# Kernel optimization log

Hardware: AMD Instinct MI355X
Metric: run time of the kernel (lower is better)

The kernel has to match this reference:

```python
import jax, jax.numpy as jnp
import numpy as np

DIM = 512
NUM_HEADS = 8
HEAD_DIM = DIM // NUM_HEADS
SCALE = HEAD_DIM ** -0.5


def setup_inputs() -> dict:
    key = jax.random.key(0)
    ks = jax.random.split(key, 5)
    B, N = 4, 2048
    x = jax.random.normal(ks[0], (B, N, DIM), dtype=jnp.float32)
    # Learned parameters (torch nn.Linear style: y = x @ W.T + b)
    w_qkv = jax.random.normal(ks[1], (3 * DIM, DIM), dtype=jnp.float32) * (DIM ** -0.5)
    b_qkv = jnp.zeros((3 * DIM,), dtype=jnp.float32)
    w_proj = jax.random.normal(ks[2], (DIM, DIM), dtype=jnp.float32) * (DIM ** -0.5)
    b_proj = jnp.zeros((DIM,), dtype=jnp.float32)
    return {"x": x, "w_qkv": w_qkv, "b_qkv": b_qkv, "w_proj": w_proj, "b_proj": b_proj}


def reference(x, w_qkv, b_qkv, w_proj, b_proj):
    B, N, C = x.shape
    qkv = x @ w_qkv.T + b_qkv                      # [B, N, 3C]
    qkv = qkv.reshape(B, N, 3, NUM_HEADS, HEAD_DIM)
    qkv = jnp.transpose(qkv, (2, 0, 3, 1, 4))      # [3, B, H, N, d]
    q, k, v = qkv[0], qkv[1], qkv[2]
    attn = jnp.einsum("bhqd,bhkd->bhqk", q, k) * SCALE  # [B, H, N, N]
    attn = jax.nn.softmax(attn, axis=-1)
    out = jnp.einsum("bhqk,bhkd->bhqd", attn, v)   # [B, H, N, d]
    out = jnp.transpose(out, (0, 2, 1, 3)).reshape(B, N, C)
    return out @ w_proj.T + b_proj
```

## Files before the change

### kernel.cpp

```cpp
#include <hip/hip_runtime.h>

#define DIM 512
#define NHEAD 8
#define HDIM 64
#define BATCH 4
#define SEQ 2048
#define MTOT (BATCH*SEQ)
#define SCALE 0.125f
#define LOG2E 1.4426950408889634f

typedef __bf16 bf16_t;
typedef __bf16 bf16x8 __attribute__((ext_vector_type(8)));
typedef __bf16 bf16x4 __attribute__((ext_vector_type(4)));
typedef __bf16 bf16x2 __attribute__((ext_vector_type(2)));
typedef float f32x4 __attribute__((ext_vector_type(4)));

#define ASYNC_COPY16(g, l) __builtin_amdgcn_global_load_lds( \
    (const __attribute__((address_space(1))) void*)(g),      \
    (__attribute__((address_space(3))) void*)(l), 16, 0, 0)

#define NX_ELEM  (4194304)
#define NWQ_ELEM (786432)
#define NWP_ELEM (262144)
__global__ __launch_bounds__(256) void cvt_kernel(const float* __restrict__ x,
                                                  const float* __restrict__ wq,
                                                  const float* __restrict__ wp,
                                                  bf16_t* __restrict__ out) {
    int i = (blockIdx.x * 256 + threadIdx.x) * 4;
    const float* src;
    if (i < NX_ELEM)                 src = x  + i;
    else if (i < NX_ELEM + NWQ_ELEM) src = wq + (i - NX_ELEM);
    else                             src = wp + (i - NX_ELEM - NWQ_ELEM);
    float4 v = *reinterpret_cast<const float4*>(src);
    bf16x4 o;
    o[0] = (bf16_t)v.x; o[1] = (bf16_t)v.y; o[2] = (bf16_t)v.z; o[3] = (bf16_t)v.w;
    *reinterpret_cast<bf16x4*>(out + i) = o;
}

__global__ __launch_bounds__(256) void gemm_qkv_kernel(
    const bf16_t* __restrict__ X, const bf16_t* __restrict__ W,
    const float* __restrict__ bias,
    bf16_t* __restrict__ Qo, bf16_t* __restrict__ Ko, bf16_t* __restrict__ Vto)
{
    __shared__ bf16_t smem[16384];
    bf16_t (*As)[64] = reinterpret_cast<bf16_t (*)[64]>(smem);
    bf16_t (*Bs)[64] = reinterpret_cast<bf16_t (*)[64]>(smem + 8192);
    unsigned int* Lw = reinterpret_cast<unsigned int*>(smem);
    const int tid = threadIdx.x;
    const int wave = tid >> 6, lane = tid & 63;
    const int lhi = lane >> 4, llo = lane & 15;
    const int o = blockIdx.x;
    const int x = o & 7, i0 = o >> 3;
    const int m0 = (x * 8 + (i0 & 7)) * 128;
    const int n0 = (i0 >> 3) * 128;
    const int wr = (wave >> 1) * 64, wc = (wave & 1) * 64;
    f32x4 acc[4][4] = {};

    const int srow = wave * 32 + (lane >> 3);
    const int scol = (lane & 7) * 8;
    const bf16_t* gA = X + (size_t)(m0 + srow) * DIM + scol;
    const bf16_t* gB = W + (size_t)(n0 + srow) * DIM + scol;

    for (int k0 = 0; k0 < DIM; k0 += 64) {
        #pragma unroll
        for (int p = 0; p < 4; ++p) {
            ASYNC_COPY16(gA + (size_t)p * 8 * DIM + k0, &As[wave*32 + p*8][0]);
            ASYNC_COPY16(gB + (size_t)p * 8 * DIM + k0, &Bs[wave*32 + p*8][0]);
        }
        __syncthreads();
        #pragma unroll
        for (int ks = 0; ks < 2; ++ks) {
            bf16x8 af[4], bfr[4];
            #pragma unroll
            for (int i = 0; i < 4; ++i)
                af[i] = *reinterpret_cast<const bf16x8*>(&As[wr + i*16 + llo][ks*32 + lhi*8]);
            #pragma unroll
            for (int j = 0; j < 4; ++j)
                bfr[j] = *reinterpret_cast<const bf16x8*>(&Bs[wc + j*16 + llo][ks*32 + lhi*8]);
            __builtin_amdgcn_s_setprio(1);
            #pragma unroll
            for (int i = 0; i < 4; ++i)
                #pragma unroll
                for (int j = 0; j < 4; ++j)
                    acc[i][j] = __builtin_amdgcn_mfma_f32_16x16x32_bf16(af[i], bfr[j], acc[i][j], 0, 0, 0);
            __builtin_amdgcn_s_setprio(0);
        }
        __syncthreads();
    }

    const int b = m0 >> 11, ns0 = m0 & 2047;

    if (n0 < 1024) {
        const float qscale = (n0 < 512) ? (SCALE * LOG2E) : 1.0f;
        bf16_t* __restrict__ dst = (n0 < 512) ? Qo : Ko;
        #pragma unroll
        for (int j = 0; j < 4; ++j) {
            int ddc = wc + j*16 + llo;
            float bv = bias[n0 + ddc];
            #pragma unroll
            for (int i = 0; i < 4; ++i)
                #pragma unroll
                for (int r = 0; r < 4; ++r) {
                    int ml = wr + i*16 + lhi*4 + r;
                    smem[ml * 128 + (ddc ^ (((ml >> 2) & 3) * 16))] =
                        (bf16_t)((acc[i][j][r] + bv) * qscale);
                }
        }
        __syncthreads();
        #pragma unroll
        for (int k = 0; k < 8; ++k) {
            int c = tid + k * 256;
            int row = c >> 4, colc = (c & 15) * 8;
            uint4 val = *reinterpret_cast<const uint4*>(
                &smem[row * 128 + (colc ^ (((row >> 2) & 3) * 16))]);
            int col = n0 + colc;
            int hh = (col >> 6) & 7, dd = col & 63;
            size_t bh = (size_t)(b * NHEAD + hh);
            *reinterpret_cast<uint4*>(dst + (bh * SEQ + ns0 + row) * HDIM + dd) = val;
        }
    } else {
        #pragma unroll
        for (int j = 0; j < 4; ++j) {
            int ddc = wc + j*16 + llo;
            float bv = bias[n0 + ddc];
            int xsw = (ddc & 7) * 4;
            #pragma unroll
            for (int i = 0; i < 4; ++i) {
                int dwb = (wr >> 1) + i*8 + lhi*2;
                #pragma unroll
                for (int r2 = 0; r2 < 2; ++r2) {
                    bf16x2 t;
                    t[0] = (bf16_t)(acc[i][j][2*r2]     + bv);
                    t[1] = (bf16_t)(acc[i][j][2*r2 + 1] + bv);
                    Lw[ddc * 64 + ((dwb + r2) ^ xsw)] = __builtin_bit_cast(unsigned int, t);
                }
            }
        }
        __syncthreads();
        const int hh_base = (n0 - 1024) >> 6;
        const int chunk = tid & 15;
        #pragma unroll
        for (int rd = 0; rd < 8; ++rd) {
            int ddc = rd * 16 + (tid >> 4);
            uint4 val = *reinterpret_cast<const uint4*>(
                &Lw[ddc * 64 + ((chunk * 4) ^ ((ddc & 7) * 4))]);
            int dd = ddc & 63;
            int hh = hh_base + (ddc >> 6);
            size_t bh = (size_t)(b * NHEAD + hh);
            *reinterpret_cast<uint4*>(Vto + (bh * HDIM + dd) * SEQ + ns0 + chunk * 8) = val;
        }
    }
}

__global__ __launch_bounds__(256, 2) void attn_kernel(
    const bf16_t* __restrict__ Q, const bf16_t* __restrict__ K,
    const bf16_t* __restrict__ Vt, bf16_t* __restrict__ O)
{
    __shared__ bf16_t Ks[2][64][64];
    __shared__ bf16_t Vs[2][64][64];
    const int tid = threadIdx.x;
    const int wave = tid >> 6, lane = tid & 63;
    const int lhi = lane >> 4, llo = lane & 15;
    const int o = blockIdx.x;
    const int w = (o & 7) * 64 + (o >> 3);
    const int qt = w & 15, bh = w >> 4;
    const bf16_t* Qb = Q + (size_t)bh * SEQ * HDIM;
    const bf16_t* Kb = K + (size_t)bh * SEQ * HDIM;
    const bf16_t* Vb = Vt + (size_t)bh * HDIM * SEQ;
    const int q0 = qt * 128 + wave * 32;

    const int ksr = tid >> 3, kg = tid & 7;
    const int kcol = (kg * 8) ^ ((ksr & 7) * 8);
    const int vd = tid >> 3, vg = tid & 7;
    const int pkA = (32*(vg>>2) + 8*((2*vg)&3)   + 4*((vg>>1)&1)) ^ ((vd & 7) * 8);
    const int pkB = (32*(vg>>2) + 8*((2*vg+1)&3) + 4*((vg>>1)&1)) ^ ((vd & 7) * 8);

    bf16x8 aq[2][2];
    #pragma unroll
    for (int qb = 0; qb < 2; ++qb)
        #pragma unroll
        for (int ks = 0; ks < 2; ++ks)
            aq[qb][ks] = *reinterpret_cast<const bf16x8*>(
                Qb + (size_t)(q0 + qb*16 + llo) * HDIM + ks*32 + lhi*8);

    bf16x8 ones;
    #pragma unroll
    for (int e = 0; e < 8; ++e) ones[e] = (bf16_t)1.0f;

    f32x4 acc_o[2][4] = {};
    f32x4 acc_l[2] = {};
    float mstat[2];
    const float THR = 8.0f * LOG2E;
    const int NT = SEQ / 64;

    uint4 kreg0, kreg1, vreg0, vreg1;
    bf16x8 apA[2][2], apB[2][2];
    bf16x8 bvA[2][4], bvB[2][4];

    auto vmax4 = [](const f32x4& v) {
        return fmaxf(fmaxf(v[0], v[1]), fmaxf(v[2], v[3]));
    };

    kreg0 = *reinterpret_cast<const uint4*>(Kb + (size_t)ksr * HDIM + kg*8);
    kreg1 = *reinterpret_cast<const uint4*>(Kb + (size_t)(ksr + 32) * HDIM + kg*8);
    vreg0 = *reinterpret_cast<const uint4*>(Vb + (size_t)vd * SEQ + vg*8);
    vreg1 = *reinterpret_cast<const uint4*>(Vb + (size_t)(vd + 32) * SEQ + vg*8);
    *reinterpret_cast<uint4*>(&Ks[0][ksr][kcol]) = kreg0;
    *reinterpret_cast<uint4*>(&Ks[0][ksr + 32][kcol]) = kreg1;
    *reinterpret_cast<uint2*>(&Vs[0][vd][pkA]) = make_uint2(vreg0.x, vreg0.y);
    *reinterpret_cast<uint2*>(&Vs[0][vd][pkB]) = make_uint2(vreg0.z, vreg0.w);
    *reinterpret_cast<uint2*>(&Vs[0][vd + 32][pkA]) = make_uint2(vreg1.x, vreg1.y);
    *reinterpret_cast<uint2*>(&Vs[0][vd + 32][pkB]) = make_uint2(vreg1.z, vreg1.w);
    __syncthreads();

    kreg0 = *reinterpret_cast<const uint4*>(Kb + (size_t)(64 + ksr) * HDIM + kg*8);
    kreg1 = *reinterpret_cast<const uint4*>(Kb + (size_t)(64 + ksr + 32) * HDIM + kg*8);
    vreg0 = *reinterpret_cast<const uint4*>(Vb + (size_t)vd * SEQ + 64 + vg*8);
    vreg1 = *reinterpret_cast<const uint4*>(Vb + (size_t)(vd + 32) * SEQ + 64 + vg*8);

    {
        f32x4 s[2][4] = {};
        __builtin_amdgcn_s_setprio(1);
        #pragma unroll
        for (int kb = 0; kb < 4; ++kb)
            #pragma unroll
            for (int ks = 0; ks < 2; ++ks) {
                bf16x8 kf = *reinterpret_cast<const bf16x8*>(
                    &Ks[0][kb*16 + llo][(ks*32 + lhi*8) ^ ((llo & 7) * 8)]);
                #pragma unroll
                for (int qb = 0; qb < 2; ++qb)
                    s[qb][kb] = __builtin_amdgcn_mfma_f32_16x16x32_bf16(kf, aq[qb][ks], s[qb][kb], 0, 0, 0);
            }
        __builtin_amdgcn_s_setprio(0);
        #pragma unroll
        for (int qb = 0; qb < 2; ++qb) {
            float mx = fmaxf(fmaxf(vmax4(s[qb][0]), vmax4(s[qb][1])),
                             fmaxf(vmax4(s[qb][2]), vmax4(s[qb][3])));
            mx = fmaxf(mx, __shfl_xor(mx, 16, 64));
            mx = fmaxf(mx, __shfl_xor(mx, 32, 64));
            mstat[qb] = mx;
            #pragma unroll
            for (int kp = 0; kp < 2; ++kp)
                #pragma unroll
                for (int j = 0; j < 4; ++j) {
                    apA[qb][kp][j]     = (bf16_t)__builtin_amdgcn_exp2f(s[qb][2*kp][j]     - mx);
                    apA[qb][kp][4 + j] = (bf16_t)__builtin_amdgcn_exp2f(s[qb][2*kp + 1][j] - mx);
                }
        }
        #pragma unroll
        for (int kp = 0; kp < 2; ++kp)
            #pragma unroll
            for (int qb = 0; qb < 2; ++qb)
                acc_l[qb] = __builtin_amdgcn_mfma_f32_16x16x32_bf16(apA[qb][kp], ones, acc_l[qb], 0, 0, 0);
        #pragma unroll
        for (int kp = 0; kp < 2; ++kp)
            #pragma unroll
            for (int db = 0; db < 4; ++db)
                bvA[kp][db] = *reinterpret_cast<const bf16x8*>(
                    &Vs[0][db*16 + llo][(kp*32 + lhi*8) ^ ((llo & 7) * 8)]);
        *reinterpret_cast<uint4*>(&Ks[1][ksr][kcol]) = kreg0;
        *reinterpret_cast<uint4*>(&Ks[1][ksr + 32][kcol]) = kreg1;
        *reinterpret_cast<uint2*>(&Vs[1][vd][pkA]) = make_uint2(vreg0.x, vreg0.y);
        *reinterpret_cast<uint2*>(&Vs[1][vd][pkB]) = make_uint2(vreg0.z, vreg0.w);
        *reinterpret_cast<uint2*>(&Vs[1][vd + 32][pkA]) = make_uint2(vreg1.x, vreg1.y);
        *reinterpret_cast<uint2*>(&Vs[1][vd + 32][pkB]) = make_uint2(vreg1.z, vreg1.w);
        __syncthreads();
    }

    auto body = [&](int kt, bf16x8 (&apIn)[2][2], bf16x8 (&bvIn)[2][4],
                    bf16x8 (&apOut)[2][2], bf16x8 (&bvOut)[2][4]) {
        const int cur = kt & 1, nxt = cur ^ 1;
        if (kt + 1 < NT) {
            const size_t koff = (size_t)(kt + 1) * 64;
            kreg0 = *reinterpret_cast<const uint4*>(Kb + (koff + ksr) * HDIM + kg*8);
            kreg1 = *reinterpret_cast<const uint4*>(Kb + (koff + ksr + 32) * HDIM + kg*8);
            vreg0 = *reinterpret_cast<const uint4*>(Vb + (size_t)vd * SEQ + koff + vg*8);
            vreg1 = *reinterpret_cast<const uint4*>(Vb + (size_t)(vd + 32) * SEQ + koff + vg*8);
        }
        f32x4 s[2][4] = {};
        __builtin_amdgcn_s_setprio(1);
        #pragma unroll
        for (int kb = 0; kb < 4; ++kb)
            #pragma unroll
            for (int ks = 0; ks < 2; ++ks) {
                bf16x8 kf = *reinterpret_cast<const bf16x8*>(
                    &Ks[cur][kb*16 + llo][(ks*32 + lhi*8) ^ ((llo & 7) * 8)]);
                #pragma unroll
                for (int qb = 0; qb < 2; ++qb)
                    s[qb][kb] = __builtin_amdgcn_mfma_f32_16x16x32_bf16(kf, aq[qb][ks], s[qb][kb], 0, 0, 0);
            }
        __builtin_amdgcn_s_setprio(0);

        float lmax[2];
        bool ok = true;
        #pragma unroll
        for (int qb = 0; qb < 2; ++qb) {
            float mx = fmaxf(fmaxf(vmax4(s[qb][0]), vmax4(s[qb][1])),
                             fmaxf(vmax4(s[qb][2]), vmax4(s[qb][3])));
            lmax[qb] = mx;
            ok &= (mx <= mstat[qb] + THR);
        }
        if (!__all(ok)) {
            #pragma unroll
            for (int kp = 0; kp < 2; ++kp)
                #pragma unroll
                for (int db = 0; db < 4; ++db)
                    #pragma unroll
                    for (int qb = 0; qb < 2; ++qb)
                        acc_o[qb][db] = __builtin_amdgcn_mfma_f32_16x16x32_bf16(apIn[qb][kp], bvIn[kp][db], acc_o[qb][db], 0, 0, 0);
            #pragma unroll
            for (int kp = 0; kp < 2; ++kp)
                #pragma unroll
                for (int db = 0; db < 4; ++db)
                    #pragma unroll
                    for (int e = 0; e < 8; ++e) bvIn[kp][db][e] = (bf16_t)0.f;
            #pragma unroll
            for (int qb = 0; qb < 2; ++qb) {
                float mx = lmax[qb];
                mx = fmaxf(mx, __shfl_xor(mx, 16, 64));
                mx = fmaxf(mx, __shfl_xor(mx, 32, 64));
                float mold = mstat[qb];
                float mn = fmaxf(mold, mx);
                float alpha = __builtin_amdgcn_exp2f(mold - mn);
                mstat[qb] = mn;
                #pragma unroll
                for (int r = 0; r < 4; ++r) {
                    float av = __shfl(alpha, (lane & 48) >> 2 | r, 64);
                    acc_l[qb][r] *= av;
                    #pragma unroll
                    for (int db = 0; db < 4; ++db) acc_o[qb][db][r] *= av;
                }
            }
        }

        __builtin_amdgcn_s_setprio(1);
        #pragma unroll
        for (int kp = 0; kp < 2; ++kp) {
            #pragma unroll
            for (int qb = 0; qb < 2; ++qb)
                #pragma unroll
                for (int j = 0; j < 4; ++j) {
                    apOut[qb][kp][j]     = (bf16_t)__builtin_amdgcn_exp2f(s[qb][2*kp][j]     - mstat[qb]);
                    apOut[qb][kp][4 + j] = (bf16_t)__builtin_amdgcn_exp2f(s[qb][2*kp + 1][j] - mstat[qb]);
                }
            #pragma unroll
            for (int db = 0; db < 4; ++db)
                #pragma unroll
                for (int qb = 0; qb < 2; ++qb)
                    acc_o[qb][db] = __builtin_amdgcn_mfma_f32_16x16x32_bf16(apIn[qb][kp], bvIn[kp][db], acc_o[qb][db], 0, 0, 0);
            #pragma unroll
            for (int qb = 0; qb < 2; ++qb)
                acc_l[qb] = __builtin_amdgcn_mfma_f32_16x16x32_bf16(apOut[qb][kp], ones, acc_l[qb], 0, 0, 0);
        }
        __builtin_amdgcn_s_setprio(0);

        #pragma unroll
        for (int kp = 0; kp < 2; ++kp)
            #pragma unroll
            for (int db = 0; db < 4; ++db)
                bvOut[kp][db] = *reinterpret_cast<const bf16x8*>(
                    &Vs[cur][db*16 + llo][(kp*32 + lhi*8) ^ ((llo & 7) * 8)]);

        if (kt + 1 < NT) {
            *reinterpret_cast<uint4*>(&Ks[nxt][ksr][kcol]) = kreg0;
            *reinterpret_cast<uint4*>(&Ks[nxt][ksr + 32][kcol]) = kreg1;
            *reinterpret_cast<uint2*>(&Vs[nxt][vd][pkA]) = make_uint2(vreg0.x, vreg0.y);
            *reinterpret_cast<uint2*>(&Vs[nxt][vd][pkB]) = make_uint2(vreg0.z, vreg0.w);
            *reinterpret_cast<uint2*>(&Vs[nxt][vd + 32][pkA]) = make_uint2(vreg1.x, vreg1.y);
            *reinterpret_cast<uint2*>(&Vs[nxt][vd + 32][pkB]) = make_uint2(vreg1.z, vreg1.w);
        }
        __syncthreads();
    };

    for (int tp = 1; tp + 1 < NT; tp += 2) {
        body(tp,     apA, bvA, apB, bvB);
        body(tp + 1, apB, bvB, apA, bvA);
    }
    body(NT - 1, apA, bvA, apB, bvB);

    #pragma unroll
    for (int kp = 0; kp < 2; ++kp)
        #pragma unroll
        for (int db = 0; db < 4; ++db)
            #pragma unroll
            for (int qb = 0; qb < 2; ++qb)
                acc_o[qb][db] = __builtin_amdgcn_mfma_f32_16x16x32_bf16(apB[qb][kp], bvB[kp][db], acc_o[qb][db], 0, 0, 0);

    const int b = bh >> 3, h = bh & 7;
    #pragma unroll
    for (int qb = 0; qb < 2; ++qb) {
        #pragma unroll
        for (int r = 0; r < 4; ++r) {
            float iv = 1.0f / acc_l[qb][r];
            int q = q0 + qb*16 + lhi*4 + r;
            #pragma unroll
            for (int db = 0; db < 4; ++db)
                O[(size_t)(b * SEQ + q) * DIM + h*HDIM + db*16 + llo] =
                    (bf16_t)(acc_o[qb][db][r] * iv);
        }
    }
}

__global__ __launch_bounds__(256) void gemm_proj_kernel(
    const bf16_t* __restrict__ X, const bf16_t* __restrict__ W,
    const float* __restrict__ bias, float* __restrict__ out)
{
    __shared__ bf16_t As[128][64];
    __shared__ bf16_t Bs[64][64];
    const int tid = threadIdx.x;
    const int wave = tid >> 6, lane = tid & 63;
    const int lhi = lane >> 4, llo = lane & 15;
    const int o = blockIdx.x;
    const int x = o & 7, i0 = o >> 3;
    const int m0 = (x * 8 + (i0 & 7)) * 128;
    const int n0 = (i0 >> 3) * 64;
    const int wr = (wave >> 1) * 64, wc = (wave & 1) * 32;
    f32x4 acc[4][2] = {};

    const int srow = wave * 32 + (lane >> 3);
    const int srowB = wave * 16 + (lane >> 3);
    const int scol = (lane & 7) * 8;
    const bf16_t* gA = X + (size_t)(m0 + srow) * DIM + scol;
    const bf16_t* gB = W + (size_t)(n0 + srowB) * DIM + scol;

    for (int k0 = 0; k0 < DIM; k0 += 64) {
        #pragma unroll
        for (int p = 0; p < 4; ++p)
            ASYNC_COPY16(gA + (size_t)p * 8 * DIM + k0, &As[wave*32 + p*8][0]);
        #pragma unroll
        for (int p = 0; p < 2; ++p)
            ASYNC_COPY16(gB + (size_t)p * 8 * DIM + k0, &Bs[wave*16 + p*8][0]);
        __syncthreads();
        #pragma unroll
        for (int ks = 0; ks < 2; ++ks) {
            bf16x8 af[4], bfr[2];
            #pragma unroll
            for (int i = 0; i < 4; ++i)
                af[i] = *reinterpret_cast<const bf16x8*>(&As[wr + i*16 + llo][ks*32 + lhi*8]);
            #pragma unroll
            for (int j = 0; j < 2; ++j)
                bfr[j] = *reinterpret_cast<const bf16x8*>(&Bs[wc + j*16 + llo][ks*32 + lhi*8]);
            __builtin_amdgcn_s_setprio(1);
            #pragma unroll
            for (int i = 0; i < 4; ++i)
                #pragma unroll
                for (int j = 0; j < 2; ++j)
                    acc[i][j] = __builtin_amdgcn_mfma_f32_16x16x32_bf16(af[i], bfr[j], acc[i][j], 0, 0, 0);
            __builtin_amdgcn_s_setprio(0);
        }
        __syncthreads();
    }

    #pragma unroll
    for (int j = 0; j < 2; ++j) {
        int col = n0 + wc + j*16 + llo;
        float bv = bias[col];
        #pragma unroll
        for (int i = 0; i < 4; ++i)
            #pragma unroll
            for (int r = 0; r < 4; ++r) {
                int m = m0 + wr + i*16 + lhi*4 + r;
                out[(size_t)m * DIM + col] = acc[i][j][r] + bv;
            }
    }
}

extern "C" void kernel_launch(void* const* d_in, const int* in_sizes, int n_in,
                              void* d_out, int out_size, void* d_ws, size_t ws_size,
                              hipStream_t stream) {
    const float* x      = (const float*)d_in[0];
    const float* w_qkv  = (const float*)d_in[1];
    const float* b_qkv  = (const float*)d_in[2];
    const float* w_proj = (const float*)d_in[3];
    const float* b_proj = (const float*)d_in[4];
    float* out = (float*)d_out;

    const size_t NX  = (size_t)MTOT * DIM;
    const size_t NWQ = (size_t)3 * DIM * DIM;
    const size_t NWP = (size_t)DIM * DIM;
    const size_t NQ  = (size_t)BATCH * NHEAD * SEQ * HDIM;

    bf16_t* Xb    = (bf16_t*)d_ws;
    bf16_t* Wqkv  = Xb + NX;
    bf16_t* Wproj = Wqkv + NWQ;
    bf16_t* Qb    = Wproj + NWP;
    bf16_t* Kb    = Qb + NQ;
    bf16_t* Vtb   = Kb + NQ;
    bf16_t* AOb   = Vtb + NQ;

    cvt_kernel<<<(int)((NX + NWQ + NWP) / 1024), 256, 0, stream>>>(x, w_qkv, w_proj, Xb);

    gemm_qkv_kernel<<<768, 256, 0, stream>>>(Xb, Wqkv, b_qkv, Qb, Kb, Vtb);

    attn_kernel<<<512, 256, 0, stream>>>(Qb, Kb, Vtb, AOb);

    gemm_proj_kernel<<<512, 256, 0, stream>>>(AOb, Wproj, b_proj, out);
}
```

Baseline: 90.30 us.

## Split attention KV range in two and merge partials in a separate kernel

The attention kernel now splits each query tile's key/value sequence into two halves, which doubles the grid from 512 to 1024 blocks. Each block writes unnormalized fp32 partial outputs plus max and sum statistics, and a new merge kernel combines the two halves into bf16 output. The launch bound is raised to request 4 blocks per SM so that more work runs at once. In exchange it adds fp32 partial-output traffic to global memory, an extra kernel launch, and possible register pressure from the tighter occupancy target.

```diff
diff --git a/kernel.cpp b/kernel.cpp
--- a/kernel.cpp
+++ b/kernel.cpp
@@ -152,9 +152,10 @@
     }
 }
 
-__global__ __launch_bounds__(256, 2) void attn_kernel(
+__global__ __launch_bounds__(256, 4) void attn_split_kernel(
     const bf16_t* __restrict__ Q, const bf16_t* __restrict__ K,
-    const bf16_t* __restrict__ Vt, bf16_t* __restrict__ O)
+    const bf16_t* __restrict__ Vt,
+    float* __restrict__ OP, float* __restrict__ MS, float* __restrict__ LS)
 {
     __shared__ bf16_t Ks[2][64][64];
     __shared__ bf16_t Vs[2][64][64];
@@ -162,12 +163,14 @@
     const int wave = tid >> 6, lane = tid & 63;
     const int lhi = lane >> 4, llo = lane & 15;
     const int o = blockIdx.x;
-    const int w = (o & 7) * 64 + (o >> 3);
-    const int qt = w & 15, bh = w >> 4;
+    const int w = (o & 7) * 128 + (o >> 3);
+    const int split = w & 1, qt = (w >> 1) & 15, bh = w >> 5;
     const bf16_t* Qb = Q + (size_t)bh * SEQ * HDIM;
     const bf16_t* Kb = K + (size_t)bh * SEQ * HDIM;
     const bf16_t* Vb = Vt + (size_t)bh * HDIM * SEQ;
     const int q0 = qt * 128 + wave * 32;
+    const size_t KOFF = (size_t)split * 1024;
+    const int NTL = 16;
 
     const int ksr = tid >> 3, kg = tid & 7;
     const int kcol = (kg * 8) ^ ((ksr & 7) * 8);
@@ -191,7 +194,6 @@
     f32x4 acc_l[2] = {};
     float mstat[2];
     const float THR = 8.0f * LOG2E;
-    const int NT = SEQ / 64;
 
     uint4 kreg0, kreg1, vreg0, vreg1;
     bf16x8 apA[2][2], apB[2][2];
@@ -201,10 +203,10 @@
         return fmaxf(fmaxf(v[0], v[1]), fmaxf(v[2], v[3]));
     };
 
-    kreg0 = *reinterpret_cast<const uint4*>(Kb + (size_t)ksr * HDIM + kg*8);
-    kreg1 = *reinterpret_cast<const uint4*>(Kb + (size_t)(ksr + 32) * HDIM + kg*8);
-    vreg0 = *reinterpret_cast<const uint4*>(Vb + (size_t)vd * SEQ + vg*8);
-    vreg1 = *reinterpret_cast<const uint4*>(Vb + (size_t)(vd + 32) * SEQ + vg*8);
+    kreg0 = *reinterpret_cast<const uint4*>(Kb + (KOFF + ksr) * HDIM + kg*8);
+    kreg1 = *reinterpret_cast<const uint4*>(Kb + (KOFF + ksr + 32) * HDIM + kg*8);
+    vreg0 = *reinterpret_cast<const uint4*>(Vb + (size_t)vd * SEQ + KOFF + vg*8);
+    vreg1 = *reinterpret_cast<const uint4*>(Vb + (size_t)(vd + 32) * SEQ + KOFF + vg*8);
     *reinterpret_cast<uint4*>(&Ks[0][ksr][kcol]) = kreg0;
     *reinterpret_cast<uint4*>(&Ks[0][ksr + 32][kcol]) = kreg1;
     *reinterpret_cast<uint2*>(&Vs[0][vd][pkA]) = make_uint2(vreg0.x, vreg0.y);
@@ -213,10 +215,10 @@
     *reinterpret_cast<uint2*>(&Vs[0][vd + 32][pkB]) = make_uint2(vreg1.z, vreg1.w);
     __syncthreads();
 
-    kreg0 = *reinterpret_cast<const uint4*>(Kb + (size_t)(64 + ksr) * HDIM + kg*8);
-    kreg1 = *reinterpret_cast<const uint4*>(Kb + (size_t)(64 + ksr + 32) * HDIM + kg*8);
-    vreg0 = *reinterpret_cast<const uint4*>(Vb + (size_t)vd * SEQ + 64 + vg*8);
-    vreg1 = *reinterpret_cast<const uint4*>(Vb + (size_t)(vd + 32) * SEQ + 64 + vg*8);
+    kreg0 = *reinterpret_cast<const uint4*>(Kb + (KOFF + 64 + ksr) * HDIM + kg*8);
+    kreg1 = *reinterpret_cast<const uint4*>(Kb + (KOFF + 64 + ksr + 32) * HDIM + kg*8);
+    vreg0 = *reinterpret_cast<const uint4*>(Vb + (size_t)vd * SEQ + KOFF + 64 + vg*8);
+    vreg1 = *reinterpret_cast<const uint4*>(Vb + (size_t)(vd + 32) * SEQ + KOFF + 64 + vg*8);
 
     {
         f32x4 s[2][4] = {};
@@ -267,11 +269,11 @@
         __syncthreads();
     }
 
-    auto body = [&](int kt, bf16x8 (&apIn)[2][2], bf16x8 (&bvIn)[2][4],
+    auto body = [&](int lt, bf16x8 (&apIn)[2][2], bf16x8 (&bvIn)[2][4],
                     bf16x8 (&apOut)[2][2], bf16x8 (&bvOut)[2][4]) {
-        const int cur = kt & 1, nxt = cur ^ 1;
-        if (kt + 1 < NT) {
-            const size_t koff = (size_t)(kt + 1) * 64;
+        const int cur = lt & 1, nxt = cur ^ 1;
+        if (lt + 1 < NTL) {
+            const size_t koff = KOFF + (size_t)(lt + 1) * 64;
             kreg0 = *reinterpret_cast<const uint4*>(Kb + (koff + ksr) * HDIM + kg*8);
             kreg1 = *reinterpret_cast<const uint4*>(Kb + (koff + ksr + 32) * HDIM + kg*8);
             vreg0 = *reinterpret_cast<const uint4*>(Vb + (size_t)vd * SEQ + koff + vg*8);
@@ -361,7 +363,7 @@
                 bvOut[kp][db] = *reinterpret_cast<const bf16x8*>(
                     &Vs[cur][db*16 + llo][(kp*32 + lhi*8) ^ ((llo & 7) * 8)]);
 
-        if (kt + 1 < NT) {
+        if (lt + 1 < NTL) {
             *reinterpret_cast<uint4*>(&Ks[nxt][ksr][kcol]) = kreg0;
             *reinterpret_cast<uint4*>(&Ks[nxt][ksr + 32][kcol]) = kreg1;
             *reinterpret_cast<uint2*>(&Vs[nxt][vd][pkA]) = make_uint2(vreg0.x, vreg0.y);
@@ -372,11 +374,11 @@
         __syncthreads();
     };
 
-    for (int tp = 1; tp + 1 < NT; tp += 2) {
+    for (int tp = 1; tp + 1 < NTL; tp += 2) {
         body(tp,     apA, bvA, apB, bvB);
         body(tp + 1, apB, bvB, apA, bvA);
     }
-    body(NT - 1, apA, bvA, apB, bvB);
+    body(NTL - 1, apA, bvA, apB, bvB);
 
     #pragma unroll
     for (int kp = 0; kp < 2; ++kp)
@@ -386,19 +388,48 @@
             for (int qb = 0; qb < 2; ++qb)
                 acc_o[qb][db] = __builtin_amdgcn_mfma_f32_16x16x32_bf16(apB[qb][kp], bvB[kp][db], acc_o[qb][db], 0, 0, 0);
 
-    const int b = bh >> 3, h = bh & 7;
+    float* op = OP + (((size_t)split * 32 + bh) * SEQ) * HDIM;
     #pragma unroll
     for (int qb = 0; qb < 2; ++qb) {
         #pragma unroll
         for (int r = 0; r < 4; ++r) {
-            float iv = 1.0f / acc_l[qb][r];
             int q = q0 + qb*16 + lhi*4 + r;
             #pragma unroll
             for (int db = 0; db < 4; ++db)
-                O[(size_t)(b * SEQ + q) * DIM + h*HDIM + db*16 + llo] =
-                    (bf16_t)(acc_o[qb][db][r] * iv);
-        }
-    }
+                op[(size_t)q * HDIM + db*16 + llo] = acc_o[qb][db][r];
+        }
+        if (lhi == 0)
+            MS[((size_t)split * 32 + bh) * SEQ + q0 + qb*16 + llo] = mstat[qb];
+        if (llo == 0)
+            #pragma unroll
+            for (int r = 0; r < 4; ++r)
+                LS[((size_t)split * 32 + bh) * SEQ + q0 + qb*16 + lhi*4 + r] = acc_l[qb][r];
+    }
+}
+
+__global__ __launch_bounds__(256) void merge_kernel(
+    const float* __restrict__ OP, const float* __restrict__ MS,
+    const float* __restrict__ LS, bf16_t* __restrict__ O)
+{
+    const int t = blockIdx.x * 256 + threadIdx.x;
+    const int dq = t & 15, q = (t >> 4) & 2047, bh = t >> 15;
+    const size_t r0 = (size_t)bh * SEQ + q;
+    const size_t r1 = (size_t)(32 + bh) * SEQ + q;
+    float m0 = MS[r0], m1 = MS[r1];
+    float l0 = LS[r0], l1 = LS[r1];
+    float M = fmaxf(m0, m1);
+    float w0 = __builtin_amdgcn_exp2f(m0 - M);
+    float w1 = __builtin_amdgcn_exp2f(m1 - M);
+    float inv = 1.0f / (w0 * l0 + w1 * l1);
+    float4 o0 = *reinterpret_cast<const float4*>(OP + r0 * HDIM + dq * 4);
+    float4 o1 = *reinterpret_cast<const float4*>(OP + r1 * HDIM + dq * 4);
+    bf16x4 res;
+    res[0] = (bf16_t)((o0.x * w0 + o1.x * w1) * inv);
+    res[1] = (bf16_t)((o0.y * w0 + o1.y * w1) * inv);
+    res[2] = (bf16_t)((o0.z * w0 + o1.z * w1) * inv);
+    res[3] = (bf16_t)((o0.w * w0 + o1.w * w1) * inv);
+    const int b = bh >> 3, h = bh & 7;
+    *reinterpret_cast<bf16x4*>(O + ((size_t)(b * SEQ + q) * DIM + h * HDIM + dq * 4)) = res;
 }
 
 __global__ __launch_bounds__(256) void gemm_proj_kernel(
@@ -487,12 +518,17 @@
     bf16_t* Kb    = Qb + NQ;
     bf16_t* Vtb   = Kb + NQ;
     bf16_t* AOb   = Vtb + NQ;
+    float*  OP    = (float*)(AOb + NQ);
+    float*  MS    = OP + 2 * NQ;
+    float*  LS    = MS + 2 * 32 * SEQ;
 
     cvt_kernel<<<(int)((NX + NWQ + NWP) / 1024), 256, 0, stream>>>(x, w_qkv, w_proj, Xb);
 
     gemm_qkv_kernel<<<768, 256, 0, stream>>>(Xb, Wqkv, b_qkv, Qb, Kb, Vtb);
 
-    attn_kernel<<<512, 256, 0, stream>>>(Qb, Kb, Vtb, AOb);
+    attn_split_kernel<<<1024, 256, 0, stream>>>(Qb, Kb, Vtb, OP, MS, LS);
+
+    merge_kernel<<<4096, 256, 0, stream>>>(OP, MS, LS, AOb);
 
     gemm_proj_kernel<<<512, 256, 0, stream>>>(AOb, Wproj, b_proj, out);
 }
```

New measurement: 324.1 us. +258.9%, slower.
